# Optimization experiments

Hardware: AMD Instinct MI355X
Metric: run time of the kernel (lower is better)

The kernel has to match this reference:

```python
import jax, jax.numpy as jnp
import numpy as np

N, E = 50000, 1600000
F_IN, F_EDGE, HID = 128, 16, 64
SLOPE = 0.2
EPS_BN = 1e-5


def setup_inputs() -> dict:
    key = jax.random.key(0)
    ks = jax.random.split(key, 24)
    g = lambda k, shp, s=0.1: (jax.random.normal(k, shp, dtype=jnp.float32) * s)
    inp = {
        'x': jax.random.normal(ks[0], (N, F_IN), dtype=jnp.float32),
        'edge_index': jax.random.randint(ks[1], (2, E), 0, N, dtype=jnp.int64),
        'edge_attr': jax.random.normal(ks[2], (E, F_EDGE), dtype=jnp.float32),
        # conv1: F_IN -> HID, 4 heads, concat
        'W1': g(ks[3], (F_IN, 4 * HID)), 'a1s': g(ks[4], (4, HID)), 'a1d': g(ks[5], (4, HID)), 'b1': jnp.zeros((4 * HID,), jnp.float32),
        # conv2: 4*HID -> HID, 4 heads, concat
        'W2': g(ks[6], (4 * HID, 4 * HID)), 'a2s': g(ks[7], (4, HID)), 'a2d': g(ks[8], (4, HID)), 'b2': jnp.zeros((4 * HID,), jnp.float32),
        # conv3: 4*HID -> HID, 1 head
        'W3': g(ks[9], (4 * HID, HID)), 'a3s': g(ks[10], (1, HID)), 'a3d': g(ks[11], (1, HID)), 'b3': jnp.zeros((HID,), jnp.float32),
        'bn1_g': jnp.ones((4 * HID,), jnp.float32), 'bn1_b': jnp.zeros((4 * HID,), jnp.float32),
        'bn2_g': jnp.ones((4 * HID,), jnp.float32), 'bn2_b': jnp.zeros((4 * HID,), jnp.float32),
        'mlp_W1': g(ks[12], (F_EDGE, HID)), 'mlp_b1': jnp.zeros((HID,), jnp.float32),
        'mlp_W2': g(ks[13], (HID, HID)), 'mlp_b2': jnp.zeros((HID,), jnp.float32),
        'fc_W': g(ks[14], (3 * HID, 1)), 'fc_b': jnp.zeros((1,), jnp.float32),
    }
    return inp


def _gat(x, W, a_s, a_d, b, src, dst, heads, dout):
    n = x.shape[0]
    h = (x @ W).reshape(n, heads, dout)                    # [N,H,D]
    ls = jnp.sum(h * a_s, axis=-1)                         # [N,H]
    ld = jnp.sum(h * a_d, axis=-1)
    logits = jax.nn.leaky_relu(ls[src] + ld[dst], SLOPE)   # [E',H]
    m = jax.ops.segment_max(logits, dst, num_segments=n)
    m = jnp.where(jnp.isfinite(m), m, 0.0)
    p = jnp.exp(logits - m[dst])
    s = jax.ops.segment_sum(p, dst, num_segments=n)
    alpha = p / (s[dst] + 1e-16)                           # segment softmax over in-edges
    out = jax.ops.segment_sum(h[src] * alpha[:, :, None], dst, num_segments=n)
    return out.reshape(n, heads * dout) + b


def _bn(x, g, b):
    mu = jnp.mean(x, axis=0)
    var = jnp.var(x, axis=0)
    return (x - mu) * jax.lax.rsqrt(var + EPS_BN) * g + b


def reference(x, edge_index, edge_attr, W1, a1s, a1d, b1, W2, a2s, a2d, b2,
              W3, a3s, a3d, b3, bn1_g, bn1_b, bn2_g, bn2_b,
              mlp_W1, mlp_b1, mlp_W2, mlp_b2, fc_W, fc_b):
    src0, dst0 = edge_index[0], edge_index[1]
    loop = jnp.arange(x.shape[0], dtype=edge_index.dtype)  # PyG adds self-loops
    src = jnp.concatenate([src0, loop])
    dst = jnp.concatenate([dst0, loop])

    h = _gat(x, W1, a1s, a1d, b1, src, dst, 4, HID)
    h = _bn(jax.nn.elu(h), bn1_g, bn1_b)
    h = _gat(h, W2, a2s, a2d, b2, src, dst, 4, HID)
    h = _bn(jax.nn.elu(h), bn2_g, bn2_b)
    h = _gat(h, W3, a3s, a3d, b3, src, dst, 1, HID)        # [N,HID]

    ef = jax.nn.relu(edge_attr @ mlp_W1 + mlp_b1) @ mlp_W2 + mlp_b2  # [E,HID]
    emb = jnp.concatenate([h[src0], h[dst0], ef], axis=1)  # [E,3*HID]
    return (emb @ fc_W + fc_b).squeeze(-1)
```

## Files before the change

### kernel.cpp

```cpp
#include <hip/hip_runtime.h>
#include <hip/hip_fp16.h>
#include <math.h>


#define FIN 128
#define HID 64
#define BIN_SHIFT 8

typedef _Float16 f16x8 __attribute__((ext_vector_type(8)));
typedef float f32x4 __attribute__((ext_vector_type(4)));

__device__ __forceinline__ unsigned short f2hbits(float f) {
    __half h = __float2half(f);
    return *reinterpret_cast<unsigned short*>(&h);
}
__device__ __forceinline__ float2 hpair(unsigned w) {
    __half2 h = *reinterpret_cast<__half2*>(&w);
    return __half22float2(h);
}

__device__ __forceinline__ unsigned fenc(float f) {
    unsigned b = __float_as_uint(f);
    return (b & 0x80000000u) ? ~b : (b | 0x80000000u);
}
__device__ __forceinline__ float fdec(unsigned k) {
    unsigned b = (k & 0x80000000u) ? (k ^ 0x80000000u) : ~k;
    return __uint_as_float(b);
}


__global__ __launch_bounds__(256) void bincount_kernel(const int* __restrict__ ei,
                                                       int* __restrict__ bincnt,
                                                       int E, int Etot) {
    __shared__ int h[256];
    int t = threadIdx.x;
    h[t] = 0;
    __syncthreads();
    int base = blockIdx.x * 4096;
    #pragma unroll
    for (int i = 0; i < 16; ++i) {
        int e = base + i * 256 + t;
        if (e < Etot) {
            int d = (e < E) ? ei[E + e] : (e - E);
            atomicAdd(&h[d >> BIN_SHIFT], 1);
        }
    }
    __syncthreads();
    if (h[t]) atomicAdd(&bincnt[t], h[t]);
}

__global__ void scanbins_kernel(const int* __restrict__ bincnt, int* __restrict__ binptr,
                                int* __restrict__ bincur, int NB, int Etot) {
    __shared__ int buf[256];
    int t = threadIdx.x;
    int v = (t < NB) ? bincnt[t] : 0;
    buf[t] = v;
    __syncthreads();
    for (int o = 1; o < 256; o <<= 1) {
        int y = (t >= o) ? buf[t - o] : 0;
        __syncthreads();
        buf[t] += y;
        __syncthreads();
    }
    int excl = buf[t] - v;
    if (t < NB) {
        binptr[t] = excl;
        bincur[t] = excl;
    }
    if (t == 0) binptr[NB] = Etot;
}

__global__ __launch_bounds__(256) void binscatter_kernel(const int* __restrict__ ei,
                                                         int* __restrict__ bincur,
                                                         int2* __restrict__ binned,
                                                         int E, int Etot) {
    __shared__ int h[256];
    __shared__ int gb[256];
    int t = threadIdx.x;
    h[t] = 0;
    __syncthreads();
    int base = blockIdx.x * 4096;
    #pragma unroll
    for (int i = 0; i < 16; ++i) {
        int e = base + i * 256 + t;
        if (e < Etot) {
            int d = (e < E) ? ei[E + e] : (e - E);
            atomicAdd(&h[d >> BIN_SHIFT], 1);
        }
    }
    __syncthreads();
    int cnt = h[t];
    if (cnt) gb[t] = atomicAdd(&bincur[t], cnt);
    __syncthreads();
    h[t] = 0;
    __syncthreads();
    #pragma unroll
    for (int i = 0; i < 16; ++i) {
        int e = base + i * 256 + t;
        if (e < Etot) {
            int s, d;
            if (e < E) { s = ei[e]; d = ei[E + e]; }
            else       { s = e - E; d = e - E; }
            int b = d >> BIN_SHIFT;
            int pos = gb[b] + atomicAdd(&h[b], 1);
            binned[pos] = make_int2(s, d);
        }
    }
}

__global__ __launch_bounds__(256) void bincsr_kernel(const int2* __restrict__ binned,
                                                     const int* __restrict__ binptr,
                                                     int* __restrict__ row_ptr,
                                                     int* __restrict__ col,
                                                     int N, int Etot) {
    __shared__ int h[256];
    __shared__ int cur[256];
    __shared__ int wsum[4];
    int b = blockIdx.x;
    int t = threadIdx.x;
    int lo = b << BIN_SHIFT;
    h[t] = 0;
    __syncthreads();
    int ebeg = binptr[b], eend = binptr[b + 1];
    for (int i = ebeg + t; i < eend; i += 256) atomicAdd(&h[binned[i].y - lo], 1);
    __syncthreads();
    int v = h[t];
    int lane = t & 63, w = t >> 6;
    int x = v;
    #pragma unroll
    for (int o = 1; o < 64; o <<= 1) {
        int y = __shfl_up(x, o);
        if (lane >= o) x += y;
    }
    if (lane == 63) wsum[w] = x;
    __syncthreads();
    int off = 0;
    #pragma unroll
    for (int i = 0; i < 4; ++i) off += (i < w) ? wsum[i] : 0;
    int excl = ebeg + off + x - v;
    int node = lo + t;
    if (node < N) row_ptr[node] = excl;
    cur[t] = excl;
    if (b == 0 && t == 0) row_ptr[N] = Etot;
    __syncthreads();
    for (int i = ebeg + t; i < eend; i += 256) {
        int2 sd = binned[i];
        int pos = atomicAdd(&cur[sd.y - lo], 1);
        col[pos] = sd.x;
    }
}


__global__ __launch_bounds__(256) void mfma_gemm_kernel(
    const float* __restrict__ X, const float* __restrict__ W,
    unsigned short* __restrict__ Yh, int Nrows, int K, int M,
    const float* __restrict__ bnsum, const float* __restrict__ bng,
    const float* __restrict__ bnb, float invN,
    const float* __restrict__ as_, const float* __restrict__ ad_,
    float* __restrict__ ls, float* __restrict__ ld,
    unsigned* __restrict__ lsmax_g, int H) {
    __shared__ __align__(16) unsigned short a_lds[128][40];
    __shared__ __align__(16) unsigned short b_lds[64][40];
    __shared__ __align__(16) float scale_l[256];
    __shared__ __align__(16) float shift_l[256];
    __shared__ unsigned lmax_l;
    const int t = threadIdx.x;
    const int row0 = blockIdx.x * 128;
    const int by = blockIdx.y;
    const int c0 = by * 64;
    const int w = t >> 6, lane = t & 63;
    const int quad = lane >> 4, mrow = lane & 15;
    if (t == 0) lmax_l = 0;
    if (bnsum && t < 256) {
        float mu = bnsum[t] * invN;
        float var = bnsum[256 + t] * invN - mu * mu;
        float sc = bng[t] * rsqrtf(var + 1e-5f);
        scale_l[t] = sc;
        shift_l[t] = bnb[t] - mu * sc;
    }
    __syncthreads();
    f32x4 acc[2][4] = {};
    for (int k0 = 0; k0 < K; k0 += 32) {
        #pragma unroll
        for (int i = 0; i < 4; ++i) {
            int f = i * 256 + t;
            int r = f >> 3, kq = f & 7;
            int grow = row0 + r;
            float4 xv = make_float4(0.f, 0.f, 0.f, 0.f);
            if (grow < Nrows) xv = *(const float4*)(X + (size_t)grow * K + k0 + kq * 4);
            if (bnsum) {
                float4 sc = *(const float4*)&scale_l[k0 + kq * 4];
                float4 sh = *(const float4*)&shift_l[k0 + kq * 4];
                xv.x = fmaf(xv.x, sc.x, sh.x);
                xv.y = fmaf(xv.y, sc.y, sh.y);
                xv.z = fmaf(xv.z, sc.z, sh.z);
                xv.w = fmaf(xv.w, sc.w, sh.w);
            }
            ushort4 pk;
            pk.x = f2hbits(xv.x);
            pk.y = f2hbits(xv.y);
            pk.z = f2hbits(xv.z);
            pk.w = f2hbits(xv.w);
            *(ushort4*)&a_lds[r][kq * 4] = pk;
        }
        #pragma unroll
        for (int i = 0; i < 2; ++i) {
            int f = i * 256 + t;
            int kr = f >> 4, cq = f & 15;
            float4 wv = *(const float4*)(W + (size_t)(k0 + kr) * M + c0 + cq * 4);
            b_lds[cq * 4 + 0][kr] = f2hbits(wv.x);
            b_lds[cq * 4 + 1][kr] = f2hbits(wv.y);
            b_lds[cq * 4 + 2][kr] = f2hbits(wv.z);
            b_lds[cq * 4 + 3][kr] = f2hbits(wv.w);
        }
        __syncthreads();
        f16x8 a0 = *(const f16x8*)&a_lds[w * 32 + mrow][quad * 8];
        f16x8 a1 = *(const f16x8*)&a_lds[w * 32 + 16 + mrow][quad * 8];
        #pragma unroll
        for (int c = 0; c < 4; ++c) {
            f16x8 bf = *(const f16x8*)&b_lds[c * 16 + mrow][quad * 8];
            acc[0][c] = __builtin_amdgcn_mfma_f32_16x16x32_f16(a0, bf, acc[0][c], 0, 0, 0);
            acc[1][c] = __builtin_amdgcn_mfma_f32_16x16x32_f16(a1, bf, acc[1][c], 0, 0, 0);
        }
        __syncthreads();
    }
    #pragma unroll
    for (int i = 0; i < 2; ++i) {
        #pragma unroll
        for (int c = 0; c < 4; ++c) {
            #pragma unroll
            for (int r = 0; r < 4; ++r) {
                int grow = row0 + w * 32 + i * 16 + quad * 4 + r;
                if (grow < Nrows)
                    Yh[(size_t)grow * M + c0 + c * 16 + mrow] = f2hbits(acc[i][c][r]);
            }
        }
    }
    float asv[4], adv[4];
    #pragma unroll
    for (int c = 0; c < 4; ++c) {
        asv[c] = as_[by * 64 + c * 16 + mrow];
        adv[c] = ad_[by * 64 + c * 16 + mrow];
    }
    float lmax = -3.0e38f;
    #pragma unroll
    for (int i = 0; i < 2; ++i) {
        #pragma unroll
        for (int r = 0; r < 4; ++r) {
            float ps = 0.f, pd = 0.f;
            #pragma unroll
            for (int c = 0; c < 4; ++c) {
                ps = fmaf(acc[i][c][r], asv[c], ps);
                pd = fmaf(acc[i][c][r], adv[c], pd);
            }
            #pragma unroll
            for (int o = 1; o <= 8; o <<= 1) {
                ps += __shfl_xor(ps, o);
                pd += __shfl_xor(pd, o);
            }
            int grow = row0 + w * 32 + i * 16 + quad * 4 + r;
            if (mrow == 0 && grow < Nrows) {
                ls[(size_t)grow * H + by] = ps;
                ld[(size_t)grow * H + by] = pd;
                lmax = fmaxf(lmax, ps);
            }
        }
    }
    if (mrow == 0) atomicMax(&lmax_l, fenc(lmax));
    __syncthreads();
    if (t == 0) atomicMax(&lsmax_g[by], lmax_l);
}


#define ACC8(hv, p)                                              \
    {                                                            \
        float2 fa = hpair((hv).x), fb = hpair((hv).y);           \
        float2 fc = hpair((hv).z), fd = hpair((hv).w);           \
        a0 = fmaf((p), fa.x, a0); a1 = fmaf((p), fa.y, a1);      \
        a2 = fmaf((p), fb.x, a2); a3 = fmaf((p), fb.y, a3);      \
        a4 = fmaf((p), fc.x, a4); a5 = fmaf((p), fc.y, a5);      \
        a6 = fmaf((p), fd.x, a6); a7 = fmaf((p), fd.y, a7);      \
    }

__global__ __launch_bounds__(256) void agg_bn_kernel(
    const unsigned short* __restrict__ hb, const float* __restrict__ ls,
    const float* __restrict__ ld, const int* __restrict__ row_ptr,
    const int* __restrict__ col, const float* __restrict__ bias,
    const unsigned* __restrict__ lsmax_g, float* __restrict__ out,
    float* __restrict__ bnsum, int N, int ngroups) {
    __shared__ float accs[4][256];
    __shared__ float accq[4][256];
    const int t = threadIdx.x;
    const int w = t >> 6, lane = t & 63;
    const int half = lane >> 5;
    const int il = lane & 31;
    const int hd = il >> 3;
    const int c0 = il * 8;
    const char* hbb = (const char*)hb;
    const char* lsc = (const char*)ls;
    const unsigned cb = (unsigned)c0 * 2u;
    const unsigned hd4 = (unsigned)hd * 4u;
    if (half == 0) {
        #pragma unroll
        for (int i = 0; i < 8; ++i) { accs[w][c0 + i] = 0.f; accq[w][c0 + i] = 0.f; }
    }
    const float lsm = fdec(lsmax_g[hd]);
    const float4 bv0 = *(const float4*)(bias + c0);
    const float4 bv1 = *(const float4*)(bias + c0 + 4);
    for (int g = blockIdx.x; g < ngroups; g += gridDim.x) {
        int n = g * 4 + w;
        if (n >= N) continue;
        int beg = row_ptr[n], end = row_ptr[n + 1];
        float4 ldn = *(const float4*)(ld + (size_t)n * 4);
        float ldn_h = (hd == 0) ? ldn.x : (hd == 1) ? ldn.y : (hd == 2) ? ldn.z : ldn.w;
        float m_h = fmaxf(0.f, ldn_h + lsm);
        float psum = 0.f;
        float a0 = 0.f, a1 = 0.f, a2 = 0.f, a3 = 0.f;
        float a4 = 0.f, a5 = 0.f, a6 = 0.f, a7 = 0.f;
        for (int base = beg; base < end; base += 64) {
            int el = base + lane;
            int s_r = (el < end) ? col[el] : 0;
            int cnt = min(64, end - base);
            int j = 0;
            for (; j + 8 <= cnt; j += 8) {
                int s0 = __shfl(s_r, j + half);
                int s1 = __shfl(s_r, j + 2 + half);
                int s2 = __shfl(s_r, j + 4 + half);
                int s3 = __shfl(s_r, j + 6 + half);
                uint4 h0 = *(const uint4*)(hbb + ((unsigned)s0 * 512u + cb));
                uint4 h1 = *(const uint4*)(hbb + ((unsigned)s1 * 512u + cb));
                uint4 h2 = *(const uint4*)(hbb + ((unsigned)s2 * 512u + cb));
                uint4 h3 = *(const uint4*)(hbb + ((unsigned)s3 * 512u + cb));
                float l0 = *(const float*)(lsc + ((unsigned)s0 * 16u + hd4));
                float l1 = *(const float*)(lsc + ((unsigned)s1 * 16u + hd4));
                float l2 = *(const float*)(lsc + ((unsigned)s2 * 16u + hd4));
                float l3 = *(const float*)(lsc + ((unsigned)s3 * 16u + hd4));
                float g0 = l0 + ldn_h; g0 = fmaxf(g0, 0.2f * g0);
                float g1 = l1 + ldn_h; g1 = fmaxf(g1, 0.2f * g1);
                float g2 = l2 + ldn_h; g2 = fmaxf(g2, 0.2f * g2);
                float g3 = l3 + ldn_h; g3 = fmaxf(g3, 0.2f * g3);
                float p0 = __expf(g0 - m_h), p1 = __expf(g1 - m_h);
                float p2 = __expf(g2 - m_h), p3 = __expf(g3 - m_h);
                psum += (p0 + p1) + (p2 + p3);
                ACC8(h0, p0) ACC8(h1, p1) ACC8(h2, p2) ACC8(h3, p3)
            }
            for (; j < cnt; j += 2) {
                int jj = j + half;
                int sj = __shfl(s_r, jj);
                bool valid = jj < cnt;
                uint4 hv = *(const uint4*)(hbb + ((unsigned)sj * 512u + cb));
                float lv = *(const float*)(lsc + ((unsigned)sj * 16u + hd4));
                float gg = lv + ldn_h; gg = fmaxf(gg, 0.2f * gg);
                float pv = valid ? __expf(gg - m_h) : 0.f;
                psum += pv;
                ACC8(hv, pv)
            }
        }
        psum += __shfl_xor(psum, 32);
        a0 += __shfl_xor(a0, 32); a1 += __shfl_xor(a1, 32);
        a2 += __shfl_xor(a2, 32); a3 += __shfl_xor(a3, 32);
        a4 += __shfl_xor(a4, 32); a5 += __shfl_xor(a5, 32);
        a6 += __shfl_xor(a6, 32); a7 += __shfl_xor(a7, 32);
        if (half == 0) {
            float inv = 1.f / (psum + 1e-16f);
            float o0 = fmaf(a0, inv, bv0.x);
            float o1 = fmaf(a1, inv, bv0.y);
            float o2 = fmaf(a2, inv, bv0.z);
            float o3 = fmaf(a3, inv, bv0.w);
            float o4 = fmaf(a4, inv, bv1.x);
            float o5 = fmaf(a5, inv, bv1.y);
            float o6 = fmaf(a6, inv, bv1.z);
            float o7 = fmaf(a7, inv, bv1.w);
            o0 = (o0 > 0.f) ? o0 : expm1f(o0);
            o1 = (o1 > 0.f) ? o1 : expm1f(o1);
            o2 = (o2 > 0.f) ? o2 : expm1f(o2);
            o3 = (o3 > 0.f) ? o3 : expm1f(o3);
            o4 = (o4 > 0.f) ? o4 : expm1f(o4);
            o5 = (o5 > 0.f) ? o5 : expm1f(o5);
            o6 = (o6 > 0.f) ? o6 : expm1f(o6);
            o7 = (o7 > 0.f) ? o7 : expm1f(o7);
            float* orow = out + (size_t)n * 256 + c0;
            *(float4*)orow = make_float4(o0, o1, o2, o3);
            *(float4*)(orow + 4) = make_float4(o4, o5, o6, o7);
            accs[w][c0 + 0] += o0; accq[w][c0 + 0] += o0 * o0;
            accs[w][c0 + 1] += o1; accq[w][c0 + 1] += o1 * o1;
            accs[w][c0 + 2] += o2; accq[w][c0 + 2] += o2 * o2;
            accs[w][c0 + 3] += o3; accq[w][c0 + 3] += o3 * o3;
            accs[w][c0 + 4] += o4; accq[w][c0 + 4] += o4 * o4;
            accs[w][c0 + 5] += o5; accq[w][c0 + 5] += o5 * o5;
            accs[w][c0 + 6] += o6; accq[w][c0 + 6] += o6 * o6;
            accs[w][c0 + 7] += o7; accq[w][c0 + 7] += o7 * o7;
        }
    }
    __syncthreads();
    float s = accs[0][t] + accs[1][t] + accs[2][t] + accs[3][t];
    float q = accq[0][t] + accq[1][t] + accq[2][t] + accq[3][t];
    atomicAdd(&bnsum[t], s);
    atomicAdd(&bnsum[256 + t], q);
}


__global__ __launch_bounds__(256) void agg3_kernel(
    const unsigned short* __restrict__ hb, const float* __restrict__ ls,
    const float* __restrict__ ld, const int* __restrict__ row_ptr,
    const int* __restrict__ col, const float* __restrict__ bias,
    const float* __restrict__ fcW, float* __restrict__ up, float* __restrict__ vp,
    const unsigned* __restrict__ lsmax_g, int N) {
    int lane = threadIdx.x & 63;
    int n = blockIdx.x * 4 + (threadIdx.x >> 6);
    if (n >= N) return;
    int beg = row_ptr[n], end = row_ptr[n + 1];
    float ldn = ld[n];
    float m_h = fmaxf(0.f, ldn + fdec(lsmax_g[0]));
    int g = lane >> 3;
    int li = lane & 7;
    int c0 = li * 8;
    const char* hbb = (const char*)hb;
    const unsigned cb = (unsigned)c0 * 2u;
    float psum = 0.f;
    float a0 = 0.f, a1 = 0.f, a2 = 0.f, a3 = 0.f;
    float a4 = 0.f, a5 = 0.f, a6 = 0.f, a7 = 0.f;
    for (int j = beg + g; j < end; j += 8) {
        int s = col[j];
        uint4 hv = *(const uint4*)(hbb + ((unsigned)s * 128u + cb));
        float lg = ls[s] + ldn;
        lg = fmaxf(lg, 0.2f * lg);
        float pv = __expf(lg - m_h);
        psum += pv;
        ACC8(hv, pv)
    }
    #pragma unroll
    for (int o = 8; o <= 32; o <<= 1) {
        psum += __shfl_xor(psum, o);
        a0 += __shfl_xor(a0, o); a1 += __shfl_xor(a1, o);
        a2 += __shfl_xor(a2, o); a3 += __shfl_xor(a3, o);
        a4 += __shfl_xor(a4, o); a5 += __shfl_xor(a5, o);
        a6 += __shfl_xor(a6, o); a7 += __shfl_xor(a7, o);
    }
    float inv = 1.f / (psum + 1e-16f);
    float v0 = fmaf(a0, inv, bias[c0 + 0]);
    float v1 = fmaf(a1, inv, bias[c0 + 1]);
    float v2 = fmaf(a2, inv, bias[c0 + 2]);
    float v3 = fmaf(a3, inv, bias[c0 + 3]);
    float v4 = fmaf(a4, inv, bias[c0 + 4]);
    float v5 = fmaf(a5, inv, bias[c0 + 5]);
    float v6 = fmaf(a6, inv, bias[c0 + 6]);
    float v7 = fmaf(a7, inv, bias[c0 + 7]);
    float pu = v0 * fcW[c0] + v1 * fcW[c0 + 1] + v2 * fcW[c0 + 2] + v3 * fcW[c0 + 3] +
               v4 * fcW[c0 + 4] + v5 * fcW[c0 + 5] + v6 * fcW[c0 + 6] + v7 * fcW[c0 + 7];
    float pv2 = v0 * fcW[64 + c0] + v1 * fcW[64 + c0 + 1] + v2 * fcW[64 + c0 + 2] +
                v3 * fcW[64 + c0 + 3] + v4 * fcW[64 + c0 + 4] + v5 * fcW[64 + c0 + 5] +
                v6 * fcW[64 + c0 + 6] + v7 * fcW[64 + c0 + 7];
    #pragma unroll
    for (int o = 1; o <= 4; o <<= 1) {
        pu += __shfl_xor(pu, o);
        pv2 += __shfl_xor(pv2, o);
    }
    if (lane == 0) {
        up[n] = pu;
        vp[n] = pv2;
    }
}


__global__ __launch_bounds__(256) void edge_out_kernel(
    const int* __restrict__ ei, const float* __restrict__ ea,
    const float* __restrict__ W1, const float* __restrict__ b1,
    const float* __restrict__ mlpW2, const float* __restrict__ mlpb2,
    const float* __restrict__ fcW, const float* __restrict__ fcb,
    const float* __restrict__ u, const float* __restrict__ v,
    float* __restrict__ out, int E) {
    __shared__ __align__(16) float W1T[64][16];
    __shared__ float w2fl[64];
    __shared__ float b1l[64];
    __shared__ float c2l;
    int t = threadIdx.x;
    for (int p = t; p < 1024; p += 256) {
        int i = p >> 6, j = p & 63;
        W1T[j][i] = W1[i * 64 + j];
    }
    if (t < 64) {
        float s = 0.f;
        for (int k = 0; k < 64; ++k) s = fmaf(mlpW2[t * 64 + k], fcW[128 + k], s);
        w2fl[t] = s;
        b1l[t] = b1[t];
    }
    if (t == 0) {
        float c = fcb[0];
        for (int k = 0; k < 64; ++k) c = fmaf(mlpb2[k], fcW[128 + k], c);
        c2l = c;
    }
    __syncthreads();
    int base = blockIdx.x * 1024;
    float eav[4][16];
    int sidx[4], didx[4];
    bool ok[4];
    #pragma unroll
    for (int k = 0; k < 4; ++k) {
        int e = base + k * 256 + t;
        ok[k] = e < E;
        int ec = ok[k] ? e : 0;
        sidx[k] = ei[ec];
        didx[k] = ei[E + ec];
        const float4* ear = (const float4*)(ea + (size_t)ec * 16);
        float4 q0 = ear[0], q1 = ear[1], q2 = ear[2], q3 = ear[3];
        eav[k][0] = q0.x;  eav[k][1] = q0.y;  eav[k][2] = q0.z;  eav[k][3] = q0.w;
        eav[k][4] = q1.x;  eav[k][5] = q1.y;  eav[k][6] = q1.z;  eav[k][7] = q1.w;
        eav[k][8] = q2.x;  eav[k][9] = q2.y;  eav[k][10] = q2.z; eav[k][11] = q2.w;
        eav[k][12] = q3.x; eav[k][13] = q3.y; eav[k][14] = q3.z; eav[k][15] = q3.w;
    }
    float acc[4] = {0.f, 0.f, 0.f, 0.f};
    #pragma unroll 4
    for (int j = 0; j < 64; ++j) {
        const float4* wr = (const float4*)&W1T[j][0];
        float4 w0 = wr[0], w1 = wr[1], w2 = wr[2], w3 = wr[3];
        float wrow[16] = {w0.x, w0.y, w0.z, w0.w, w1.x, w1.y, w1.z, w1.w,
                          w2.x, w2.y, w2.z, w2.w, w3.x, w3.y, w3.z, w3.w};
        float bj = b1l[j], wj = w2fl[j];
        #pragma unroll
        for (int k = 0; k < 4; ++k) {
            float s = bj;
            #pragma unroll
            for (int q = 0; q < 16; ++q) s = fmaf(eav[k][q], wrow[q], s);
            s = fmaxf(s, 0.f);
            acc[k] = fmaf(s, wj, acc[k]);
        }
    }
    float cc = c2l;
    #pragma unroll
    for (int k = 0; k < 4; ++k) {
        if (ok[k]) {
            int e = base + k * 256 + t;
            out[e] = u[sidx[k]] + v[didx[k]] + acc[k] + cc;
        }
    }
}


extern "C" void kernel_launch(void* const* d_in, const int* in_sizes, int n_in,
                              void* d_out, int out_size, void* d_ws, size_t ws_size,
                              hipStream_t stream) {
    const float* x     = (const float*)d_in[0];
    const int*   ei    = (const int*)d_in[1];
    const float* ea    = (const float*)d_in[2];
    const float* W1    = (const float*)d_in[3];
    const float* a1s   = (const float*)d_in[4];
    const float* a1d   = (const float*)d_in[5];
    const float* b1    = (const float*)d_in[6];
    const float* W2    = (const float*)d_in[7];
    const float* a2s   = (const float*)d_in[8];
    const float* a2d   = (const float*)d_in[9];
    const float* b2    = (const float*)d_in[10];
    const float* W3    = (const float*)d_in[11];
    const float* a3s   = (const float*)d_in[12];
    const float* a3d   = (const float*)d_in[13];
    const float* b3    = (const float*)d_in[14];
    const float* bn1g  = (const float*)d_in[15];
    const float* bn1b  = (const float*)d_in[16];
    const float* bn2g  = (const float*)d_in[17];
    const float* bn2b  = (const float*)d_in[18];
    const float* mlpW1 = (const float*)d_in[19];
    const float* mlpb1 = (const float*)d_in[20];
    const float* mlpW2 = (const float*)d_in[21];
    const float* mlpb2 = (const float*)d_in[22];
    const float* fcW   = (const float*)d_in[23];
    const float* fcb   = (const float*)d_in[24];
    float* out = (float*)d_out;

    const int N = in_sizes[0] / FIN;
    const int E = in_sizes[1] / 2;
    const int Etot = E + N;
    const int NB = (N + 255) >> BIN_SHIFT;

    char* wsb = (char*)d_ws;
    size_t off = 0;
    auto alloc = [&](size_t bytes) {
        void* p = wsb + off;
        off += (bytes + 63) & ~(size_t)63;
        return p;
    };
    unsigned short* hAb = (unsigned short*)alloc((size_t)N * 256 * 2);
    float* hB  = (float*)alloc((size_t)N * 256 * 4);
    unsigned short* h3b = (unsigned short*)alloc((size_t)N * 64 * 2);
    float* lsb = (float*)alloc((size_t)N * 4 * 4);
    float* ldb = (float*)alloc((size_t)N * 4 * 4);
    int* row_ptr = (int*)alloc((size_t)(N + 1) * 4);
    int* colb    = (int*)alloc((size_t)Etot * 4);
    int2* binned = (int2*)alloc((size_t)Etot * 8);
    int* zreg    = (int*)alloc((256 + 16 + 512 + 512) * 4);
    int* bincnt  = zreg;
    unsigned* lsmax1 = (unsigned*)(zreg + 256);
    unsigned* lsmax2 = lsmax1 + 4;
    unsigned* lsmax3 = lsmax1 + 8;
    float* bnsumA = (float*)(zreg + 256 + 16);
    float* bnsumB = bnsumA + 512;
    int* binptr  = (int*)alloc((size_t)(NB + 1) * 4);
    int* bincur  = (int*)alloc((size_t)NB * 4);
    float* ub  = (float*)alloc((size_t)N * 4);
    float* vb  = (float*)alloc((size_t)N * 4);
    (void)ws_size; (void)n_in; (void)out_size;

    const int nb4 = (N + 3) / 4;
    const int nch = (Etot + 4095) / 4096;
    const float invN = 1.f / (float)N;

    hipMemsetAsync(zreg, 0, (256 + 16 + 512 + 512) * sizeof(int), stream);
    bincount_kernel<<<nch, 256, 0, stream>>>(ei, bincnt, E, Etot);
    scanbins_kernel<<<1, 256, 0, stream>>>(bincnt, binptr, bincur, NB, Etot);
    binscatter_kernel<<<nch, 256, 0, stream>>>(ei, bincur, binned, E, Etot);
    bincsr_kernel<<<NB, 256, 0, stream>>>(binned, binptr, row_ptr, colb, N, Etot);

    dim3 ggrid((N + 127) / 128, 4);
    dim3 ggrid3((N + 127) / 128, 1);

    mfma_gemm_kernel<<<ggrid, 256, 0, stream>>>(x, W1, hAb, N, 128, 256,
        nullptr, nullptr, nullptr, invN, a1s, a1d, lsb, ldb, lsmax1, 4);
    agg_bn_kernel<<<2048, 256, 0, stream>>>(hAb, lsb, ldb, row_ptr, colb, b1,
                                            lsmax1, hB, bnsumA, N, nb4);
    mfma_gemm_kernel<<<ggrid, 256, 0, stream>>>(hB, W2, hAb, N, 256, 256,
        bnsumA, bn1g, bn1b, invN, a2s, a2d, lsb, ldb, lsmax2, 4);
    agg_bn_kernel<<<2048, 256, 0, stream>>>(hAb, lsb, ldb, row_ptr, colb, b2,
                                            lsmax2, hB, bnsumB, N, nb4);
    mfma_gemm_kernel<<<ggrid3, 256, 0, stream>>>(hB, W3, h3b, N, 256, 64,
        bnsumB, bn2g, bn2b, invN, a3s, a3d, lsb, ldb, lsmax3, 1);
    agg3_kernel<<<nb4, 256, 0, stream>>>(h3b, lsb, ldb, row_ptr, colb, b3,
                                         fcW, ub, vb, lsmax3, N);
    edge_out_kernel<<<(E + 1023) / 1024, 256, 0, stream>>>(
        ei, ea, mlpW1, mlpb1, mlpW2, mlpb2, fcW, fcb, ub, vb, out, E);
}
```

Measured before the change: 751.4 us.

## Split GAT aggregation into per-XCD column slices with head-major attention logits

Rewrites the 4-head aggregation kernel so each block handles one 32-channel column slice, chosen as blockIdx mod 8. With round-robin block placement, each slice's 64-byte gathered rows should stay resident in one XCD's L2 instead of every XCD streaming the full fp16 feature matrix. Each wave now processes 8 edges in parallel with 4 channels per lane. The attention-logit arrays are stored head-major so the per-slice source-logit gathers are contiguous per head. The cost is that the CSR index and logit reads, softmax exponentials and row-pointer loads are repeated for every slice, and the gathers become narrower 8-byte loads.

```diff
diff --git a/kernel.cpp b/kernel.cpp
--- a/kernel.cpp
+++ b/kernel.cpp
@@ -170,6 +170,7 @@
     const int c0 = by * 64;
     const int w = t >> 6, lane = t & 63;
     const int quad = lane >> 4, mrow = lane & 15;
+    (void)H;
     if (t == 0) lmax_l = 0;
     if (bnsum && t < 256) {
         float mu = bnsum[t] * invN;
@@ -260,8 +261,8 @@
             }
             int grow = row0 + w * 32 + i * 16 + quad * 4 + r;
             if (mrow == 0 && grow < Nrows) {
-                ls[(size_t)grow * H + by] = ps;
-                ld[(size_t)grow * H + by] = pd;
+                ls[(size_t)by * Nrows + grow] = ps;
+                ld[(size_t)by * Nrows + grow] = pd;
                 lmax = fmaxf(lmax, ps);
             }
         }
@@ -269,6 +270,118 @@
     if (mrow == 0) atomicMax(&lmax_l, fenc(lmax));
     __syncthreads();
     if (t == 0) atomicMax(&lsmax_g[by], lmax_l);
+}
+
+
+#define ACC4(hv, p)                                              \
+    {                                                            \
+        float2 fa = hpair((hv).x), fb = hpair((hv).y);           \
+        a0 = fmaf((p), fa.x, a0); a1 = fmaf((p), fa.y, a1);      \
+        a2 = fmaf((p), fb.x, a2); a3 = fmaf((p), fb.y, a3);      \
+    }
+
+__global__ __launch_bounds__(256) void agg_bn_kernel(
+    const unsigned short* __restrict__ hb, const float* __restrict__ ls,
+    const float* __restrict__ ld, const int* __restrict__ row_ptr,
+    const int* __restrict__ col, const float* __restrict__ bias,
+    const unsigned* __restrict__ lsmax_g, float* __restrict__ out,
+    float* __restrict__ bnsum, int N) {
+    __shared__ float accs[4][32];
+    __shared__ float accq[4][32];
+    const int t = threadIdx.x;
+    const int w = t >> 6, lane = t & 63;
+    const int slice = blockIdx.x & 7;
+    const int bslice = blockIdx.x >> 3;
+    const int g = lane >> 3;
+    const int c8 = lane & 7;
+    const int hd = slice >> 1;
+    const char* hbb = (const char*)hb;
+    const float* __restrict__ lsp = ls + (size_t)hd * N;
+    const float* __restrict__ ldp = ld + (size_t)hd * N;
+    const unsigned cb = (unsigned)slice * 64u + (unsigned)c8 * 8u;
+    const float lsm = fdec(lsmax_g[hd]);
+    const int cbase = slice * 32 + c8 * 4;
+    const float4 bv = *(const float4*)(bias + cbase);
+    float bns0 = 0.f, bns1 = 0.f, bns2 = 0.f, bns3 = 0.f;
+    float bnq0 = 0.f, bnq1 = 0.f, bnq2 = 0.f, bnq3 = 0.f;
+    for (int n = bslice * 4 + w; n < N; n += 1024) {
+        int beg = row_ptr[n], end = row_ptr[n + 1];
+        float ldn_h = ldp[n];
+        float m_h = fmaxf(0.f, ldn_h + lsm);
+        float psum = 0.f;
+        float a0 = 0.f, a1 = 0.f, a2 = 0.f, a3 = 0.f;
+        for (int base = beg; base < end; base += 64) {
+            int el = base + lane;
+            int s_r = (el < end) ? col[el] : 0;
+            int cnt = min(64, end - base);
+            int j = 0;
+            for (; j + 32 <= cnt; j += 32) {
+                int sA = __shfl(s_r, j + g);
+                int sB = __shfl(s_r, j + 8 + g);
+                int sC = __shfl(s_r, j + 16 + g);
+                int sD = __shfl(s_r, j + 24 + g);
+                uint2 hA = *(const uint2*)(hbb + ((unsigned)sA * 512u + cb));
+                uint2 hB = *(const uint2*)(hbb + ((unsigned)sB * 512u + cb));
+                uint2 hC = *(const uint2*)(hbb + ((unsigned)sC * 512u + cb));
+                uint2 hD = *(const uint2*)(hbb + ((unsigned)sD * 512u + cb));
+                float lA = lsp[sA], lB = lsp[sB], lC = lsp[sC], lD = lsp[sD];
+                float gA = lA + ldn_h; gA = fmaxf(gA, 0.2f * gA);
+                float gB = lB + ldn_h; gB = fmaxf(gB, 0.2f * gB);
+                float gC = lC + ldn_h; gC = fmaxf(gC, 0.2f * gC);
+                float gD = lD + ldn_h; gD = fmaxf(gD, 0.2f * gD);
+                float pA = __expf(gA - m_h), pB = __expf(gB - m_h);
+                float pC = __expf(gC - m_h), pD = __expf(gD - m_h);
+                psum += (pA + pB) + (pC + pD);
+                ACC4(hA, pA) ACC4(hB, pB) ACC4(hC, pC) ACC4(hD, pD)
+            }
+            for (; j < cnt; j += 8) {
+                int jj = j + g;
+                int sj = __shfl(s_r, jj & 63);
+                bool valid = jj < cnt;
+                uint2 hv = *(const uint2*)(hbb + ((unsigned)sj * 512u + cb));
+                float lv = lsp[sj];
+                float gg = lv + ldn_h; gg = fmaxf(gg, 0.2f * gg);
+                float pv = valid ? __expf(gg - m_h) : 0.f;
+                psum += pv;
+                ACC4(hv, pv)
+            }
+        }
+        #pragma unroll
+        for (int o = 8; o <= 32; o <<= 1) {
+            psum += __shfl_xor(psum, o);
+            a0 += __shfl_xor(a0, o); a1 += __shfl_xor(a1, o);
+            a2 += __shfl_xor(a2, o); a3 += __shfl_xor(a3, o);
+        }
+        if (g == 0) {
+            float inv = 1.f / (psum + 1e-16f);
+            float o0 = fmaf(a0, inv, bv.x);
+            float o1 = fmaf(a1, inv, bv.y);
+            float o2 = fmaf(a2, inv, bv.z);
+            float o3 = fmaf(a3, inv, bv.w);
+            o0 = (o0 > 0.f) ? o0 : expm1f(o0);
+            o1 = (o1 > 0.f) ? o1 : expm1f(o1);
+            o2 = (o2 > 0.f) ? o2 : expm1f(o2);
+            o3 = (o3 > 0.f) ? o3 : expm1f(o3);
+            *(float4*)(out + (size_t)n * 256 + cbase) = make_float4(o0, o1, o2, o3);
+            bns0 += o0; bnq0 += o0 * o0;
+            bns1 += o1; bnq1 += o1 * o1;
+            bns2 += o2; bnq2 += o2 * o2;
+            bns3 += o3; bnq3 += o3 * o3;
+        }
+    }
+    if (g == 0) {
+        accs[w][c8 * 4 + 0] = bns0; accq[w][c8 * 4 + 0] = bnq0;
+        accs[w][c8 * 4 + 1] = bns1; accq[w][c8 * 4 + 1] = bnq1;
+        accs[w][c8 * 4 + 2] = bns2; accq[w][c8 * 4 + 2] = bnq2;
+        accs[w][c8 * 4 + 3] = bns3; accq[w][c8 * 4 + 3] = bnq3;
+    }
+    __syncthreads();
+    if (t < 32) {
+        float s = accs[0][t] + accs[1][t] + accs[2][t] + accs[3][t];
+        float q = accq[0][t] + accq[1][t] + accq[2][t] + accq[3][t];
+        atomicAdd(&bnsum[slice * 32 + t], s);
+        atomicAdd(&bnsum[256 + slice * 32 + t], q);
+    }
 }
 
 
@@ -281,124 +394,6 @@
         a4 = fmaf((p), fc.x, a4); a5 = fmaf((p), fc.y, a5);      \
         a6 = fmaf((p), fd.x, a6); a7 = fmaf((p), fd.y, a7);      \
     }
-
-__global__ __launch_bounds__(256) void agg_bn_kernel(
-    const unsigned short* __restrict__ hb, const float* __restrict__ ls,
-    const float* __restrict__ ld, const int* __restrict__ row_ptr,
-    const int* __restrict__ col, const float* __restrict__ bias,
-    const unsigned* __restrict__ lsmax_g, float* __restrict__ out,
-    float* __restrict__ bnsum, int N, int ngroups) {
-    __shared__ float accs[4][256];
-    __shared__ float accq[4][256];
-    const int t = threadIdx.x;
-    const int w = t >> 6, lane = t & 63;
-    const int half = lane >> 5;
-    const int il = lane & 31;
-    const int hd = il >> 3;
-    const int c0 = il * 8;
-    const char* hbb = (const char*)hb;
-    const char* lsc = (const char*)ls;
-    const unsigned cb = (unsigned)c0 * 2u;
-    const unsigned hd4 = (unsigned)hd * 4u;
-    if (half == 0) {
-        #pragma unroll
-        for (int i = 0; i < 8; ++i) { accs[w][c0 + i] = 0.f; accq[w][c0 + i] = 0.f; }
-    }
-    const float lsm = fdec(lsmax_g[hd]);
-    const float4 bv0 = *(const float4*)(bias + c0);
-    const float4 bv1 = *(const float4*)(bias + c0 + 4);
-    for (int g = blockIdx.x; g < ngroups; g += gridDim.x) {
-        int n = g * 4 + w;
-        if (n >= N) continue;
-        int beg = row_ptr[n], end = row_ptr[n + 1];
-        float4 ldn = *(const float4*)(ld + (size_t)n * 4);
-        float ldn_h = (hd == 0) ? ldn.x : (hd == 1) ? ldn.y : (hd == 2) ? ldn.z : ldn.w;
-        float m_h = fmaxf(0.f, ldn_h + lsm);
-        float psum = 0.f;
-        float a0 = 0.f, a1 = 0.f, a2 = 0.f, a3 = 0.f;
-        float a4 = 0.f, a5 = 0.f, a6 = 0.f, a7 = 0.f;
-        for (int base = beg; base < end; base += 64) {
-            int el = base + lane;
-            int s_r = (el < end) ? col[el] : 0;
-            int cnt = min(64, end - base);
-            int j = 0;
-            for (; j + 8 <= cnt; j += 8) {
-                int s0 = __shfl(s_r, j + half);
-                int s1 = __shfl(s_r, j + 2 + half);
-                int s2 = __shfl(s_r, j + 4 + half);
-                int s3 = __shfl(s_r, j + 6 + half);
-                uint4 h0 = *(const uint4*)(hbb + ((unsigned)s0 * 512u + cb));
-                uint4 h1 = *(const uint4*)(hbb + ((unsigned)s1 * 512u + cb));
-                uint4 h2 = *(const uint4*)(hbb + ((unsigned)s2 * 512u + cb));
-                uint4 h3 = *(const uint4*)(hbb + ((unsigned)s3 * 512u + cb));
-                float l0 = *(const float*)(lsc + ((unsigned)s0 * 16u + hd4));
-                float l1 = *(const float*)(lsc + ((unsigned)s1 * 16u + hd4));
-                float l2 = *(const float*)(lsc + ((unsigned)s2 * 16u + hd4));
-                float l3 = *(const float*)(lsc + ((unsigned)s3 * 16u + hd4));
-                float g0 = l0 + ldn_h; g0 = fmaxf(g0, 0.2f * g0);
-                float g1 = l1 + ldn_h; g1 = fmaxf(g1, 0.2f * g1);
-                float g2 = l2 + ldn_h; g2 = fmaxf(g2, 0.2f * g2);
-                float g3 = l3 + ldn_h; g3 = fmaxf(g3, 0.2f * g3);
-                float p0 = __expf(g0 - m_h), p1 = __expf(g1 - m_h);
-                float p2 = __expf(g2 - m_h), p3 = __expf(g3 - m_h);
-                psum += (p0 + p1) + (p2 + p3);
-                ACC8(h0, p0) ACC8(h1, p1) ACC8(h2, p2) ACC8(h3, p3)
-            }
-            for (; j < cnt; j += 2) {
-                int jj = j + half;
-                int sj = __shfl(s_r, jj);
-                bool valid = jj < cnt;
-                uint4 hv = *(const uint4*)(hbb + ((unsigned)sj * 512u + cb));
-                float lv = *(const float*)(lsc + ((unsigned)sj * 16u + hd4));
-                float gg = lv + ldn_h; gg = fmaxf(gg, 0.2f * gg);
-                float pv = valid ? __expf(gg - m_h) : 0.f;
-                psum += pv;
-                ACC8(hv, pv)
-            }
-        }
-        psum += __shfl_xor(psum, 32);
-        a0 += __shfl_xor(a0, 32); a1 += __shfl_xor(a1, 32);
-        a2 += __shfl_xor(a2, 32); a3 += __shfl_xor(a3, 32);
-        a4 += __shfl_xor(a4, 32); a5 += __shfl_xor(a5, 32);
-        a6 += __shfl_xor(a6, 32); a7 += __shfl_xor(a7, 32);
-        if (half == 0) {
-            float inv = 1.f / (psum + 1e-16f);
-            float o0 = fmaf(a0, inv, bv0.x);
-            float o1 = fmaf(a1, inv, bv0.y);
-            float o2 = fmaf(a2, inv, bv0.z);
-            float o3 = fmaf(a3, inv, bv0.w);
-            float o4 = fmaf(a4, inv, bv1.x);
-            float o5 = fmaf(a5, inv, bv1.y);
-            float o6 = fmaf(a6, inv, bv1.z);
-            float o7 = fmaf(a7, inv, bv1.w);
-            o0 = (o0 > 0.f) ? o0 : expm1f(o0);
-            o1 = (o1 > 0.f) ? o1 : expm1f(o1);
-            o2 = (o2 > 0.f) ? o2 : expm1f(o2);
-            o3 = (o3 > 0.f) ? o3 : expm1f(o3);
-            o4 = (o4 > 0.f) ? o4 : expm1f(o4);
-            o5 = (o5 > 0.f) ? o5 : expm1f(o5);
-            o6 = (o6 > 0.f) ? o6 : expm1f(o6);
-            o7 = (o7 > 0.f) ? o7 : expm1f(o7);
-            float* orow = out + (size_t)n * 256 + c0;
-            *(float4*)orow = make_float4(o0, o1, o2, o3);
-            *(float4*)(orow + 4) = make_float4(o4, o5, o6, o7);
-            accs[w][c0 + 0] += o0; accq[w][c0 + 0] += o0 * o0;
-            accs[w][c0 + 1] += o1; accq[w][c0 + 1] += o1 * o1;
-            accs[w][c0 + 2] += o2; accq[w][c0 + 2] += o2 * o2;
-            accs[w][c0 + 3] += o3; accq[w][c0 + 3] += o3 * o3;
-            accs[w][c0 + 4] += o4; accq[w][c0 + 4] += o4 * o4;
-            accs[w][c0 + 5] += o5; accq[w][c0 + 5] += o5 * o5;
-            accs[w][c0 + 6] += o6; accq[w][c0 + 6] += o6 * o6;
-            accs[w][c0 + 7] += o7; accq[w][c0 + 7] += o7 * o7;
-        }
-    }
-    __syncthreads();
-    float s = accs[0][t] + accs[1][t] + accs[2][t] + accs[3][t];
-    float q = accq[0][t] + accq[1][t] + accq[2][t] + accq[3][t];
-    atomicAdd(&bnsum[t], s);
-    atomicAdd(&bnsum[256 + t], q);
-}
-
 
 __global__ __launch_bounds__(256) void agg3_kernel(
     const unsigned short* __restrict__ hb, const float* __restrict__ ls,
@@ -616,11 +611,11 @@
     mfma_gemm_kernel<<<ggrid, 256, 0, stream>>>(x, W1, hAb, N, 128, 256,
         nullptr, nullptr, nullptr, invN, a1s, a1d, lsb, ldb, lsmax1, 4);
     agg_bn_kernel<<<2048, 256, 0, stream>>>(hAb, lsb, ldb, row_ptr, colb, b1,
-                                            lsmax1, hB, bnsumA, N, nb4);
+                                            lsmax1, hB, bnsumA, N);
     mfma_gemm_kernel<<<ggrid, 256, 0, stream>>>(hB, W2, hAb, N, 256, 256,
         bnsumA, bn1g, bn1b, invN, a2s, a2d, lsb, ldb, lsmax2, 4);
     agg_bn_kernel<<<2048, 256, 0, stream>>>(hAb, lsb, ldb, row_ptr, colb, b2,
-                                            lsmax2, hB, bnsumB, N, nb4);
+                                            lsmax2, hB, bnsumB, N);
     mfma_gemm_kernel<<<ggrid3, 256, 0, stream>>>(hB, W3, h3b, N, 256, 64,
         bnsumB, bn2g, bn2b, invN, a3s, a3d, lsb, ldb, lsmax3, 1);
     agg3_kernel<<<nb4, 256, 0, stream>>>(h3b, lsb, ldb, row_ptr, colb, b3,
```

Measured after the change: 1.035 ms. 1.38x slower.
